# Kernel tuning notes

Measured on AMD Instinct MI355X. Metric: run time of the kernel, lower is better.

The kernel has to match this reference:

```python
import jax, jax.numpy as jnp
import numpy as np

LN_EPS = 1e-5  # torch LayerNorm default

def _phi(x):
    # elu(x) + 1 feature map
    return jax.nn.elu(x) + 1.0

def setup_inputs() -> dict:
    key = jax.random.key(0)
    ks = jax.random.split(key, 5)
    B, N, D = 4, 8192, 1024
    s = 1.0 / np.sqrt(D)
    return {
        "H": jax.random.normal(ks[0], (B, N, D), dtype=jnp.float32),
        "W_qkv": jax.random.normal(ks[1], (3 * D, D), dtype=jnp.float32) * s,
        "b_qkv": jax.random.normal(ks[2], (3 * D,), dtype=jnp.float32) * 0.01,
        "W_proj": jax.random.normal(ks[3], (D, D), dtype=jnp.float32) * s,
        "b_proj": jax.random.normal(ks[4], (D,), dtype=jnp.float32) * 0.01,
        "gamma": jnp.ones((D,), dtype=jnp.float32),
        "beta": jnp.zeros((D,), dtype=jnp.float32),
    }

def reference(H, W_qkv, b_qkv, W_proj, b_proj, gamma, beta):
    B, N, D = H.shape
    num_heads = 16
    head_dim = D // num_heads
    residual = H
    # qkv projection: (B,N,3D)
    qkv = jnp.einsum('bnd,ed->bne', H, W_qkv) + b_qkv
    qkv = qkv.reshape(B, N, 3, num_heads, head_dim).transpose(2, 0, 3, 1, 4)
    q, k, v = qkv[0], qkv[1], qkv[2]  # each (B,h,N,d)
    q = _phi(q)
    k = _phi(k)
    # kv outer-product accumulated over nodes: (B,h,d,v)
    kv = jnp.einsum('bhnd,bhnv->bhdv', k, v)
    k1 = k.sum(axis=2)  # (B,h,d)
    qkv_out = jnp.einsum('bhnd,bhdv->bhnv', q, kv)
    qk1 = jnp.sum(q * k1[:, :, None, :], axis=-1, keepdims=True)
    out = qkv_out / jnp.clip(qk1, 1e-6, None)
    # NOTE: faithful to original -- reshape (B,h,N,d) -> (B,N,D) WITHOUT head transpose
    out = out.reshape(B, N, D)
    out = jnp.einsum('bnd,ed->bne', out, W_proj) + b_proj
    # LayerNorm over last dim
    mu = out.mean(axis=-1, keepdims=True)
    var = out.var(axis=-1, keepdims=True)
    out = (out - mu) * jax.lax.rsqrt(var + LN_EPS) * gamma + beta
    # dropout is identity at inference
    return out + residual
```

## Files before the change

### kernel.cpp

```cpp
#include <hip/hip_runtime.h>


typedef __attribute__((ext_vector_type(4))) float f32x4;
typedef __attribute__((ext_vector_type(8))) short bf16x8;

__device__ __forceinline__ unsigned short f2b(float f) {
    unsigned u = __float_as_uint(f);
    u = (u + 0x7FFFu + ((u >> 16) & 1u)) >> 16;
    return (unsigned short)u;
}
__device__ __forceinline__ float b2f(unsigned short h) {
    return __uint_as_float(((unsigned)h) << 16);
}

__device__ __forceinline__ void glds16(const void* gp, void* lp) {
    __builtin_amdgcn_global_load_lds(
        (__attribute__((address_space(1))) void*)(unsigned long long)gp,
        (__attribute__((address_space(3))) void*)(unsigned int)(unsigned long long)lp,
        16, 0, 0);
}

__global__ __launch_bounds__(256) void cvt_all(const float* __restrict__ H,
                                               const float* __restrict__ Wq,
                                               const float* __restrict__ Wp,
                                               unsigned short* __restrict__ hbf,
                                               unsigned short* __restrict__ wqb,
                                               unsigned short* __restrict__ wpb) {
    const int blk = blockIdx.x;
    const float* src; unsigned short* dst; long n4; int b0, nb;
    if (blk < 1792)      { src = H;  dst = hbf; n4 = 8388608; b0 = 0;    nb = 1792; }
    else if (blk < 1920) { src = Wq; dst = wqb; n4 = 786432;  b0 = 1792; nb = 128; }
    else                 { src = Wp; dst = wpb; n4 = 262144;  b0 = 1920; nb = 64; }
    long i = (long)(blk - b0) * 256 + threadIdx.x;
    const long stride = (long)nb * 256;
    for (; i < n4; i += stride) {
        float4 v = ((const float4*)src)[i];
        ushort4 o;
        o.x = f2b(v.x); o.y = f2b(v.y); o.z = f2b(v.z); o.w = f2b(v.w);
        ((ushort4*)dst)[i] = o;
    }
}

template<int MODE>
__global__ __launch_bounds__(512) void gemm256(const unsigned short* __restrict__ A,
                                               const unsigned short* __restrict__ B,
                                               const float* __restrict__ bias,
                                               void* __restrict__ Cout,
                                               int mb, int N, int K) {
    __shared__ unsigned short lds[2][2][256][64];
    const int tid = threadIdx.x;
    const int wid = tid >> 6, lane = tid & 63;
    const int wr = wid >> 2, wc = wid & 3;
    const int lr = lane & 15, lq = lane >> 4;
    const int cpx = (int)gridDim.x >> 3;
    const int L = ((int)blockIdx.x & 7) * cpx + ((int)blockIdx.x >> 3);
    const int nbv = N >> 8;
    const int gsz = 4 * nbv;
    const int g = L / gsz, r = L % gsz;
    const int bn = r >> 2;
    const int bm = g * 4 + (r & 3);
    const size_t aRow0 = (size_t)bm * 256, bRow0 = (size_t)bn * 256;

    const int sr8 = lane >> 3;
    const int ssw = ((lane & 7) ^ sr8) * 8;
    const unsigned short* aG = A + (aRow0 + (size_t)(wid * 8 + sr8)) * K + ssw;
    const unsigned short* bG = B + (bRow0 + (size_t)(wid * 8 + sr8)) * K + ssw;

    f32x4 acc[8][4] = {};
    const char* base = (const char*)&lds[0][0][0][0];

    auto stage = [&](int buf, int k0) {
#pragma unroll
        for (int j = 0; j < 8; ++j) {
            const unsigned short* g2 = (j < 4 ? aG : bG) + (size_t)(j & 3) * 64 * K + k0;
            glds16(g2, &lds[buf][j >> 2][(j & 3) * 64 + wid * 8][0]);
        }
    };
    auto ldA = [&](int cur, int mi, int ks) {
        int row = wr * 128 + mi * 16 + lr;
        int off = (cur * 2 + 0) * 32768 + row * 128 + ((((ks << 2) | lq) ^ (row & 7)) << 4);
        return *(const bf16x8*)(base + off);
    };
    auto ldB = [&](int cur, int ni, int ks) {
        int row = wc * 64 + ni * 16 + lr;
        int off = (cur * 2 + 1) * 32768 + row * 128 + ((((ks << 2) | lq) ^ (row & 7)) << 4);
        return *(const bf16x8*)(base + off);
    };

    const int nt = K >> 6;
    stage(0, 0);
    asm volatile("s_waitcnt vmcnt(0)" ::: "memory");
    __builtin_amdgcn_s_barrier();

    bf16x8 af[4][2], bfr[4][2];
    for (int t = 0; t < nt; ++t) {
        const int cur = t & 1;
#pragma unroll
        for (int mi = 0; mi < 4; ++mi) {
            af[mi][0] = ldA(cur, mi, 0); af[mi][1] = ldA(cur, mi, 1);
        }
#pragma unroll
        for (int ni = 0; ni < 2; ++ni) {
            bfr[ni][0] = ldB(cur, ni, 0); bfr[ni][1] = ldB(cur, ni, 1);
        }
        if (t + 1 < nt) stage(cur ^ 1, (t + 1) << 6);
        __builtin_amdgcn_s_barrier();
        __builtin_amdgcn_s_setprio(1);
#pragma unroll
        for (int mi = 0; mi < 4; ++mi)
#pragma unroll
            for (int ni = 0; ni < 2; ++ni)
#pragma unroll
                for (int ks = 0; ks < 2; ++ks)
                    acc[mi][ni] = __builtin_amdgcn_mfma_f32_16x16x32_bf16(
                        af[mi][ks], bfr[ni][ks], acc[mi][ni], 0, 0, 0);
        __builtin_amdgcn_s_setprio(0);
        __builtin_amdgcn_s_barrier();
#pragma unroll
        for (int ni = 2; ni < 4; ++ni) {
            bfr[ni][0] = ldB(cur, ni, 0); bfr[ni][1] = ldB(cur, ni, 1);
        }
        __builtin_amdgcn_s_barrier();
        __builtin_amdgcn_s_setprio(1);
#pragma unroll
        for (int mi = 0; mi < 4; ++mi)
#pragma unroll
            for (int ni = 2; ni < 4; ++ni)
#pragma unroll
                for (int ks = 0; ks < 2; ++ks)
                    acc[mi][ni] = __builtin_amdgcn_mfma_f32_16x16x32_bf16(
                        af[mi][ks], bfr[ni][ks], acc[mi][ni], 0, 0, 0);
        __builtin_amdgcn_s_setprio(0);
        __builtin_amdgcn_s_barrier();
#pragma unroll
        for (int mi = 0; mi < 4; ++mi) {
            af[mi][0] = ldA(cur, mi + 4, 0); af[mi][1] = ldA(cur, mi + 4, 1);
        }
        __builtin_amdgcn_s_barrier();
        __builtin_amdgcn_s_setprio(1);
#pragma unroll
        for (int mi = 0; mi < 4; ++mi)
#pragma unroll
            for (int ni = 2; ni < 4; ++ni)
#pragma unroll
                for (int ks = 0; ks < 2; ++ks)
                    acc[mi + 4][ni] = __builtin_amdgcn_mfma_f32_16x16x32_bf16(
                        af[mi][ks], bfr[ni][ks], acc[mi + 4][ni], 0, 0, 0);
        __builtin_amdgcn_s_setprio(0);
        __builtin_amdgcn_s_barrier();
        __builtin_amdgcn_s_setprio(1);
#pragma unroll
        for (int mi = 0; mi < 4; ++mi)
#pragma unroll
            for (int ni = 0; ni < 2; ++ni)
#pragma unroll
                for (int ks = 0; ks < 2; ++ks)
                    acc[mi + 4][ni] = __builtin_amdgcn_mfma_f32_16x16x32_bf16(
                        af[mi][ks], bfr[ni][ks], acc[mi + 4][ni], 0, 0, 0);
        __builtin_amdgcn_s_setprio(0);
        asm volatile("s_waitcnt vmcnt(0)" ::: "memory");
        __builtin_amdgcn_s_barrier();
        __builtin_amdgcn_sched_barrier(0);
    }
#pragma unroll
    for (int mi = 0; mi < 8; ++mi) {
#pragma unroll
        for (int ni = 0; ni < 4; ++ni) {
            int col = (int)bRow0 + wc * 64 + ni * 16 + lr;
            float bv = bias[col];
#pragma unroll
            for (int r2 = 0; r2 < 4; ++r2) {
                size_t row = aRow0 + wr * 128 + mi * 16 + lq * 4 + r2;
                float v = acc[mi][ni][r2] + bv;
                if (MODE == 0) {
                    if (col < 2048) v = (v > 0.f) ? (v + 1.f) : __expf(v);
                }
                ((unsigned short*)Cout)[row * (size_t)N + col] = f2b(v);
            }
        }
    }
}

__global__ __launch_bounds__(256) void kv_partial(const unsigned short* __restrict__ qkv,
                                                  float* __restrict__ part) {
    const int bh = blockIdx.x, chunk = blockIdx.y;
    const int b = bh >> 4, h = bh & 15;
    __shared__ unsigned short kb[16][64];
    __shared__ unsigned short vb[16][64];
    const int tid = threadIdx.x;
    const int d0 = (tid >> 4) * 4, v0 = (tid & 15) * 4;
    float acc[4][4] = {};
    float k1a[4] = {0.f, 0.f, 0.f, 0.f};
    const size_t base = ((size_t)b * 8192 + (size_t)chunk * 1024) * 3072;
    const int nn = tid >> 4;
    const int which = (tid >> 3) & 1;
    const int cg = tid & 7;
    const size_t loff = base + (size_t)nn * 3072 + (which ? 2048 : 1024) + h * 64 + cg * 8;

    for (int n0 = 0; n0 < 1024; n0 += 16) {
        uint4 val = *(const uint4*)(qkv + loff + (size_t)n0 * 3072);
        if (which) *(uint4*)(&vb[nn][cg * 8]) = val;
        else       *(uint4*)(&kb[nn][cg * 8]) = val;
        __syncthreads();
#pragma unroll 4
        for (int j = 0; j < 16; ++j) {
            ushort4 ku = *(const ushort4*)(&kb[j][d0]);
            ushort4 vu = *(const ushort4*)(&vb[j][v0]);
            float kd[4] = {b2f(ku.x), b2f(ku.y), b2f(ku.z), b2f(ku.w)};
            float vd[4] = {b2f(vu.x), b2f(vu.y), b2f(vu.z), b2f(vu.w)};
#pragma unroll
            for (int i = 0; i < 4; ++i)
#pragma unroll
                for (int jj = 0; jj < 4; ++jj)
                    acc[i][jj] += kd[i] * vd[jj];
            if ((tid & 15) == 0)
#pragma unroll
                for (int i = 0; i < 4; ++i) k1a[i] += kd[i];
        }
        __syncthreads();
    }
    float* dst = part + ((size_t)bh * 8 + chunk) * 4160;
#pragma unroll
    for (int i = 0; i < 4; ++i)
#pragma unroll
        for (int jj = 0; jj < 4; ++jj)
            dst[(v0 + jj) * 64 + d0 + i] = acc[i][jj];
    if ((tid & 15) == 0)
#pragma unroll
        for (int i = 0; i < 4; ++i) dst[4096 + d0 + i] = k1a[i];
}

__global__ __launch_bounds__(256) void kv_finish(const float* __restrict__ part,
                                                 unsigned short* __restrict__ kvbf,
                                                 float* __restrict__ k1f) {
    const int bh = blockIdx.x;
    const float* src = part + (size_t)bh * 8 * 4160;
    for (int i = threadIdx.x; i < 4096; i += 256) {
        float s = 0.f;
#pragma unroll
        for (int c = 0; c < 8; ++c) s += src[c * 4160 + i];
        kvbf[(size_t)bh * 4096 + i] = f2b(s);
    }
    if (threadIdx.x < 64) {
        float s = 0.f;
#pragma unroll
        for (int c = 0; c < 8; ++c) s += src[c * 4160 + 4096 + threadIdx.x];
        k1f[bh * 64 + threadIdx.x] = s;
    }
}

__global__ __launch_bounds__(256) void apply_attn(const unsigned short* __restrict__ qkv,
                                                  const unsigned short* __restrict__ kvbf,
                                                  const float* __restrict__ k1f,
                                                  unsigned short* __restrict__ att) {
    const int nblk = blockIdx.x;
    const int bh = blockIdx.y;
    const int b = bh >> 4, h = bh & 15;
    __shared__ unsigned short kvs[64][64];
    __shared__ float k1s[64];
    __shared__ float qk1s[64];
    const int tid = threadIdx.x;
    {
        const int v = tid >> 3, s = tid & 7;
        const uint4* srcv = (const uint4*)(kvbf + (size_t)bh * 4096);
#pragma unroll
        for (int half = 0; half < 2; ++half) {
            int vv = v + half * 32;
            uint4 val = srcv[vv * 8 + s];
            *(uint4*)(&kvs[vv][(s ^ (vv & 7)) * 8]) = val;
        }
        if (tid < 64) k1s[tid] = k1f[bh * 64 + tid];
    }
    __syncthreads();
    const int n0 = nblk * 64;
    const size_t qbase = ((size_t)b * 8192 + n0) * 3072 + h * 64;
    {
        const int row = tid >> 2, dq = (tid & 3) * 16;
        const unsigned short* qp = qkv + qbase + (size_t)row * 3072 + dq;
        float s = 0.f;
#pragma unroll
        for (int g2 = 0; g2 < 2; ++g2) {
            ushort4 u0 = *(const ushort4*)(qp + g2 * 8);
            ushort4 u1 = *(const ushort4*)(qp + g2 * 8 + 4);
            const float* kp = &k1s[dq + g2 * 8];
            s += b2f(u0.x) * kp[0] + b2f(u0.y) * kp[1] + b2f(u0.z) * kp[2] + b2f(u0.w) * kp[3]
               + b2f(u1.x) * kp[4] + b2f(u1.y) * kp[5] + b2f(u1.z) * kp[6] + b2f(u1.w) * kp[7];
        }
        s += __shfl_xor(s, 1, 64);
        s += __shfl_xor(s, 2, 64);
        if ((tid & 3) == 0) qk1s[row] = s;
    }
    __syncthreads();
    const int w = tid >> 6, lane = tid & 63;
    const int lr = lane & 15, lq = lane >> 4;
    bf16x8 af[2];
#pragma unroll
    for (int ks = 0; ks < 2; ++ks)
        af[ks] = *(const bf16x8*)(qkv + qbase + (size_t)(w * 16 + lr) * 3072 + ks * 32 + lq * 8);
    f32x4 acc[4] = {};
#pragma unroll
    for (int ni = 0; ni < 4; ++ni)
#pragma unroll
        for (int ks = 0; ks < 2; ++ks) {
            int v = ni * 16 + lr;
            bf16x8 bf = *(const bf16x8*)(&kvs[v][(((ks << 2) | lq) ^ (v & 7)) * 8]);
            acc[ni] = __builtin_amdgcn_mfma_f32_16x16x32_bf16(af[ks], bf, acc[ni], 0, 0, 0);
        }
    unsigned short* dstrow = att + (((size_t)b * 8192) + h * 512 + nblk * 4 + w) * 1024;
#pragma unroll
    for (int r = 0; r < 4; ++r) {
        float rinv = 1.f / fmaxf(qk1s[w * 16 + lq * 4 + r], 1e-6f);
#pragma unroll
        for (int ni = 0; ni < 4; ++ni)
            dstrow[(lq * 4 + r) * 64 + ni * 16 + lr] = f2b(acc[ni][r] * rinv);
    }
}

__global__ __launch_bounds__(256) void ln_residual(const unsigned short* __restrict__ X,
                                                   const float* __restrict__ H,
                                                   const float* __restrict__ gamma,
                                                   const float* __restrict__ beta,
                                                   float* __restrict__ out,
                                                   int nrows) {
    const int lane = threadIdx.x & 63;
    int row = blockIdx.x * 4 + (threadIdx.x >> 6);
    const int rstride = gridDim.x * 4;
    for (; row < nrows; row += rstride) {
        const unsigned short* x = X + (size_t)row * 1024;
        float v[16];
        float s = 0.f, s2 = 0.f;
#pragma unroll
        for (int j = 0; j < 4; ++j) {
            ushort4 u = *(const ushort4*)(x + j * 256 + lane * 4);
            float a = b2f(u.x), b = b2f(u.y), c = b2f(u.z), d = b2f(u.w);
            v[j * 4 + 0] = a; v[j * 4 + 1] = b; v[j * 4 + 2] = c; v[j * 4 + 3] = d;
            s += a + b + c + d;
            s2 += a * a + b * b + c * c + d * d;
        }
#pragma unroll
        for (int o = 32; o > 0; o >>= 1) {
            s  += __shfl_xor(s, o, 64);
            s2 += __shfl_xor(s2, o, 64);
        }
        const float mu = s * (1.f / 1024.f);
        const float var = s2 * (1.f / 1024.f) - mu * mu;
        const float inv = rsqrtf(var + 1e-5f);
        const float* hrow = H + (size_t)row * 1024;
        float* orow = out + (size_t)row * 1024;
#pragma unroll
        for (int j = 0; j < 4; ++j) {
            const int c = j * 256 + lane * 4;
            float4 g = *(const float4*)(gamma + c);
            float4 bt = *(const float4*)(beta + c);
            float4 hr = *(const float4*)(hrow + c);
            float4 o;
            o.x = (v[j * 4 + 0] - mu) * inv * g.x + bt.x + hr.x;
            o.y = (v[j * 4 + 1] - mu) * inv * g.y + bt.y + hr.y;
            o.z = (v[j * 4 + 2] - mu) * inv * g.z + bt.z + hr.z;
            o.w = (v[j * 4 + 3] - mu) * inv * g.w + bt.w + hr.w;
            *(float4*)(orow + c) = o;
        }
    }
}

extern "C" void kernel_launch(void* const* d_in, const int* in_sizes, int n_in,
                              void* d_out, int out_size, void* d_ws, size_t ws_size,
                              hipStream_t stream) {
    const float* H     = (const float*)d_in[0];
    const float* Wqkv  = (const float*)d_in[1];
    const float* bqkv  = (const float*)d_in[2];
    const float* Wproj = (const float*)d_in[3];
    const float* bproj = (const float*)d_in[4];
    const float* gamma = (const float*)d_in[5];
    const float* beta  = (const float*)d_in[6];
    float* out = (float*)d_out;
    char* ws = (char*)d_ws;

    unsigned short* wq_bf = (unsigned short*)(ws);
    unsigned short* wp_bf = (unsigned short*)(ws + 6291456);
    unsigned short* hbf   = (unsigned short*)(ws + 8388608);
    unsigned short* att   = hbf;
    unsigned short* qkvbf = (unsigned short*)(ws + 75497472);
    unsigned short* out2  = (unsigned short*)(ws + 75497472);
    unsigned short* kvbf  = (unsigned short*)(ws + 276824064);
    float*          k1f   = (float*)(ws + 277348352);
    float*          part  = (float*)(ws + 277889024);

    cvt_all<<<1984, 256, 0, stream>>>(H, Wqkv, Wproj, hbf, wq_bf, wp_bf);

    gemm256<0><<<1536, 512, 0, stream>>>(hbf, wq_bf, bqkv, (void*)qkvbf,
                                         128, 3072, 1024);

    kv_partial<<<dim3(64, 8), 256, 0, stream>>>(qkvbf, part);
    kv_finish<<<64, 256, 0, stream>>>(part, kvbf, k1f);

    apply_attn<<<dim3(128, 64), 256, 0, stream>>>(qkvbf, kvbf, k1f, att);

    gemm256<1><<<512, 512, 0, stream>>>(att, wp_bf, bproj, (void*)out2,
                                        128, 1024, 1024);

    ln_residual<<<2048, 256, 0, stream>>>(out2, H, gamma, beta, out, 32768);
}
```

Before: 564.0 us.

## Fuse H fp32-to-bf16 conversion into QKV GEMM A-operand staging

The separate conversion pass over H is removed. The QKV GEMM now loads fp32 H tiles into registers, converts them to bf16 and writes them into LDS during the K loop, while the weights still go through global_load_lds. This avoids writing and re-reading a 64MB bf16 copy of H, at the cost of an fp32 A stream that re-reads H once per column block of the 3072-wide output, plus more registers and VALU work inside the GEMM. kv_partial also now converts K/V to fp32 when storing them to padded LDS, so the inner loop no longer converts bf16 on every read.

```diff
diff --git a/kernel.cpp b/kernel.cpp
--- a/kernel.cpp
+++ b/kernel.cpp
@@ -20,17 +20,14 @@
         16, 0, 0);
 }
 
-__global__ __launch_bounds__(256) void cvt_all(const float* __restrict__ H,
-                                               const float* __restrict__ Wq,
-                                               const float* __restrict__ Wp,
-                                               unsigned short* __restrict__ hbf,
-                                               unsigned short* __restrict__ wqb,
-                                               unsigned short* __restrict__ wpb) {
+__global__ __launch_bounds__(256) void cvt_w(const float* __restrict__ Wq,
+                                             const float* __restrict__ Wp,
+                                             unsigned short* __restrict__ wqb,
+                                             unsigned short* __restrict__ wpb) {
     const int blk = blockIdx.x;
     const float* src; unsigned short* dst; long n4; int b0, nb;
-    if (blk < 1792)      { src = H;  dst = hbf; n4 = 8388608; b0 = 0;    nb = 1792; }
-    else if (blk < 1920) { src = Wq; dst = wqb; n4 = 786432;  b0 = 1792; nb = 128; }
-    else                 { src = Wp; dst = wpb; n4 = 262144;  b0 = 1920; nb = 64; }
+    if (blk < 128) { src = Wq; dst = wqb; n4 = 786432; b0 = 0;   nb = 128; }
+    else           { src = Wp; dst = wpb; n4 = 262144; b0 = 128; nb = 64; }
     long i = (long)(blk - b0) * 256 + threadIdx.x;
     const long stride = (long)nb * 256;
     for (; i < n4; i += stride) {
@@ -41,8 +38,8 @@
     }
 }
 
-template<int MODE>
-__global__ __launch_bounds__(512) void gemm256(const unsigned short* __restrict__ A,
+template<int MODE, int AF32>
+__global__ __launch_bounds__(512) void gemm256(const void* __restrict__ Ain,
                                                const unsigned short* __restrict__ B,
                                                const float* __restrict__ bias,
                                                void* __restrict__ Cout,
@@ -62,18 +59,45 @@
     const size_t aRow0 = (size_t)bm * 256, bRow0 = (size_t)bn * 256;
 
     const int sr8 = lane >> 3;
-    const int ssw = ((lane & 7) ^ sr8) * 8;
-    const unsigned short* aG = A + (aRow0 + (size_t)(wid * 8 + sr8)) * K + ssw;
+    const int sl = lane & 7;
+    const int ssw = (sl ^ sr8) * 8;
+    const unsigned short* aGb = (const unsigned short*)Ain
+                                + (aRow0 + (size_t)(wid * 8 + sr8)) * K + ssw;
+    const float* aGf = (const float*)Ain
+                       + (aRow0 + (size_t)(wid * 8 + sr8)) * K + ssw;
     const unsigned short* bG = B + (bRow0 + (size_t)(wid * 8 + sr8)) * K + ssw;
 
     f32x4 acc[8][4] = {};
     const char* base = (const char*)&lds[0][0][0][0];
-
-    auto stage = [&](int buf, int k0) {
-#pragma unroll
-        for (int j = 0; j < 8; ++j) {
-            const unsigned short* g2 = (j < 4 ? aG : bG) + (size_t)(j & 3) * 64 * K + k0;
-            glds16(g2, &lds[buf][j >> 2][(j & 3) * 64 + wid * 8][0]);
+    float4 areg[4][2];
+
+    auto stageB = [&](int buf, int k0) {
+#pragma unroll
+        for (int j = 0; j < 4; ++j)
+            glds16(bG + (size_t)j * 64 * K + k0, &lds[buf][1][j * 64 + wid * 8][0]);
+    };
+    auto stageAg = [&](int buf, int k0) {
+#pragma unroll
+        for (int j = 0; j < 4; ++j)
+            glds16(aGb + (size_t)j * 64 * K + k0, &lds[buf][0][j * 64 + wid * 8][0]);
+    };
+    auto loadA = [&](int k0) {
+#pragma unroll
+        for (int j = 0; j < 4; ++j) {
+            const float* src = aGf + (size_t)j * 64 * K + k0;
+            areg[j][0] = *(const float4*)(src);
+            areg[j][1] = *(const float4*)(src + 4);
+        }
+    };
+    auto writeA = [&](int buf) {
+#pragma unroll
+        for (int j = 0; j < 4; ++j) {
+            union { unsigned short us[8]; uint4 u; } o;
+            o.us[0] = f2b(areg[j][0].x); o.us[1] = f2b(areg[j][0].y);
+            o.us[2] = f2b(areg[j][0].z); o.us[3] = f2b(areg[j][0].w);
+            o.us[4] = f2b(areg[j][1].x); o.us[5] = f2b(areg[j][1].y);
+            o.us[6] = f2b(areg[j][1].z); o.us[7] = f2b(areg[j][1].w);
+            *(uint4*)(&lds[buf][0][j * 64 + wid * 8 + sr8][sl * 8]) = o.u;
         }
     };
     auto ldA = [&](int cur, int mi, int ks) {
@@ -88,9 +112,9 @@
     };
 
     const int nt = K >> 6;
-    stage(0, 0);
-    asm volatile("s_waitcnt vmcnt(0)" ::: "memory");
-    __builtin_amdgcn_s_barrier();
+    if (AF32) { loadA(0); writeA(0); stageB(0, 0); }
+    else      { stageAg(0, 0); stageB(0, 0); }
+    __syncthreads();
 
     bf16x8 af[4][2], bfr[4][2];
     for (int t = 0; t < nt; ++t) {
@@ -103,7 +127,10 @@
         for (int ni = 0; ni < 2; ++ni) {
             bfr[ni][0] = ldB(cur, ni, 0); bfr[ni][1] = ldB(cur, ni, 1);
         }
-        if (t + 1 < nt) stage(cur ^ 1, (t + 1) << 6);
+        if (t + 1 < nt) {
+            if (AF32) { loadA((t + 1) << 6); stageB(cur ^ 1, (t + 1) << 6); }
+            else      { stageAg(cur ^ 1, (t + 1) << 6); stageB(cur ^ 1, (t + 1) << 6); }
+        }
         __builtin_amdgcn_s_barrier();
         __builtin_amdgcn_s_setprio(1);
 #pragma unroll
@@ -136,6 +163,7 @@
         for (int mi = 0; mi < 4; ++mi) {
             af[mi][0] = ldA(cur, mi + 4, 0); af[mi][1] = ldA(cur, mi + 4, 1);
         }
+        if (AF32 && t + 1 < nt) writeA(cur ^ 1);
         __builtin_amdgcn_s_barrier();
         __builtin_amdgcn_s_setprio(1);
 #pragma unroll
@@ -158,7 +186,7 @@
                     acc[mi + 4][ni] = __builtin_amdgcn_mfma_f32_16x16x32_bf16(
                         af[mi][ks], bfr[ni][ks], acc[mi + 4][ni], 0, 0, 0);
         __builtin_amdgcn_s_setprio(0);
-        asm volatile("s_waitcnt vmcnt(0)" ::: "memory");
+        asm volatile("s_waitcnt vmcnt(0) lgkmcnt(0)" ::: "memory");
         __builtin_amdgcn_s_barrier();
         __builtin_amdgcn_sched_barrier(0);
     }
@@ -185,8 +213,8 @@
                                                   float* __restrict__ part) {
     const int bh = blockIdx.x, chunk = blockIdx.y;
     const int b = bh >> 4, h = bh & 15;
-    __shared__ unsigned short kb[16][64];
-    __shared__ unsigned short vb[16][64];
+    __shared__ float kbf[16][68];
+    __shared__ float vbf[16][68];
     const int tid = threadIdx.x;
     const int d0 = (tid >> 4) * 4, v0 = (tid & 15) * 4;
     float acc[4][4] = {};
@@ -199,23 +227,24 @@
 
     for (int n0 = 0; n0 < 1024; n0 += 16) {
         uint4 val = *(const uint4*)(qkv + loff + (size_t)n0 * 3072);
-        if (which) *(uint4*)(&vb[nn][cg * 8]) = val;
-        else       *(uint4*)(&kb[nn][cg * 8]) = val;
+        float* dst = (which ? &vbf[nn][0] : &kbf[nn][0]) + cg * 8;
+        const unsigned short* us = (const unsigned short*)&val;
+        float4 f0 = {b2f(us[0]), b2f(us[1]), b2f(us[2]), b2f(us[3])};
+        float4 f1 = {b2f(us[4]), b2f(us[5]), b2f(us[6]), b2f(us[7])};
+        *(float4*)(dst) = f0;
+        *(float4*)(dst + 4) = f1;
         __syncthreads();
 #pragma unroll 4
         for (int j = 0; j < 16; ++j) {
-            ushort4 ku = *(const ushort4*)(&kb[j][d0]);
-            ushort4 vu = *(const ushort4*)(&vb[j][v0]);
-            float kd[4] = {b2f(ku.x), b2f(ku.y), b2f(ku.z), b2f(ku.w)};
-            float vd[4] = {b2f(vu.x), b2f(vu.y), b2f(vu.z), b2f(vu.w)};
-#pragma unroll
-            for (int i = 0; i < 4; ++i)
-#pragma unroll
-                for (int jj = 0; jj < 4; ++jj)
-                    acc[i][jj] += kd[i] * vd[jj];
-            if ((tid & 15) == 0)
-#pragma unroll
-                for (int i = 0; i < 4; ++i) k1a[i] += kd[i];
+            float4 kd = *(const float4*)(&kbf[j][d0]);
+            float4 vd = *(const float4*)(&vbf[j][v0]);
+            acc[0][0] += kd.x * vd.x; acc[0][1] += kd.x * vd.y; acc[0][2] += kd.x * vd.z; acc[0][3] += kd.x * vd.w;
+            acc[1][0] += kd.y * vd.x; acc[1][1] += kd.y * vd.y; acc[1][2] += kd.y * vd.z; acc[1][3] += kd.y * vd.w;
+            acc[2][0] += kd.z * vd.x; acc[2][1] += kd.z * vd.y; acc[2][2] += kd.z * vd.z; acc[2][3] += kd.z * vd.w;
+            acc[3][0] += kd.w * vd.x; acc[3][1] += kd.w * vd.y; acc[3][2] += kd.w * vd.z; acc[3][3] += kd.w * vd.w;
+            if ((tid & 15) == 0) {
+                k1a[0] += kd.x; k1a[1] += kd.y; k1a[2] += kd.z; k1a[3] += kd.w;
+            }
         }
         __syncthreads();
     }
@@ -378,26 +407,25 @@
 
     unsigned short* wq_bf = (unsigned short*)(ws);
     unsigned short* wp_bf = (unsigned short*)(ws + 6291456);
-    unsigned short* hbf   = (unsigned short*)(ws + 8388608);
-    unsigned short* att   = hbf;
+    unsigned short* att   = (unsigned short*)(ws + 8388608);
     unsigned short* qkvbf = (unsigned short*)(ws + 75497472);
     unsigned short* out2  = (unsigned short*)(ws + 75497472);
     unsigned short* kvbf  = (unsigned short*)(ws + 276824064);
     float*          k1f   = (float*)(ws + 277348352);
     float*          part  = (float*)(ws + 277889024);
 
-    cvt_all<<<1984, 256, 0, stream>>>(H, Wqkv, Wproj, hbf, wq_bf, wp_bf);
-
-    gemm256<0><<<1536, 512, 0, stream>>>(hbf, wq_bf, bqkv, (void*)qkvbf,
-                                         128, 3072, 1024);
+    cvt_w<<<192, 256, 0, stream>>>(Wqkv, Wproj, wq_bf, wp_bf);
+
+    gemm256<0, 1><<<1536, 512, 0, stream>>>((const void*)H, wq_bf, bqkv,
+                                            (void*)qkvbf, 128, 3072, 1024);
 
     kv_partial<<<dim3(64, 8), 256, 0, stream>>>(qkvbf, part);
     kv_finish<<<64, 256, 0, stream>>>(part, kvbf, k1f);
 
     apply_attn<<<dim3(128, 64), 256, 0, stream>>>(qkvbf, kvbf, k1f, att);
 
-    gemm256<1><<<512, 512, 0, stream>>>(att, wp_bf, bproj, (void*)out2,
-                                        128, 1024, 1024);
+    gemm256<1, 0><<<512, 512, 0, stream>>>((const void*)att, wp_bf, bproj,
+                                           (void*)out2, 128, 1024, 1024);
 
     ln_residual<<<2048, 256, 0, stream>>>(out2, H, gamma, beta, out, 32768);
 }
```

After: 712.3 us. 1.26x slower.
